# Optimization experiments

Hardware: AMD Instinct MI355X
Metric: run time of the kernel (lower is better)

Reference implementation:

```python
import jax, jax.numpy as jnp
import numpy as np

TAU = 1.0
LOSS_WEIGHT = 1.0
N = 4_000_000


def setup_inputs() -> dict:
    key = jax.random.key(0)
    k1, k2 = jax.random.split(key)

    def make_boxes(k):
        u = jax.random.uniform(k, (N, 5), dtype=jnp.float32)
        xy = u[:, :2] * 1024.0                 # centers in a 1024px image
        wh = u[:, 2:4] * 100.0 + 4.0           # box sizes in [4, 104)
        r = (u[:, 4:5] - 0.5) * jnp.pi         # angle in [-pi/2, pi/2)
        return jnp.concatenate([xy, wh, r], axis=-1)

    return {"pred": make_boxes(k1), "target": make_boxes(k2)}


def xy_wh_r_2_xy_sigma(xywhr):
    """(N,5) rbox -> (mu (N,2), sigma (N,2,2)) via R @ (S/2)^2 @ R^T closed form."""
    xy = xywhr[..., :2]
    wh = jnp.clip(xywhr[..., 2:4], 1e-7, 1e7)
    r = xywhr[..., 4]
    c, s = jnp.cos(r), jnp.sin(r)
    a = (0.5 * wh[..., 0]) ** 2  # (w/2)^2
    b = (0.5 * wh[..., 1]) ** 2  # (h/2)^2
    s00 = a * c * c + b * s * s
    s11 = a * s * s + b * c * c
    s01 = (a - b) * s * c
    sigma = jnp.stack(
        [jnp.stack([s00, s01], -1), jnp.stack([s01, s11], -1)], -2
    )  # (N,2,2)
    return xy, sigma


def _det2(m):
    return m[..., 0, 0] * m[..., 1, 1] - m[..., 0, 1] * m[..., 1, 0]


def _inv2(m):
    det = _det2(m)
    adj = jnp.stack(
        [jnp.stack([m[..., 1, 1], -m[..., 0, 1]], -1),
         jnp.stack([-m[..., 1, 0], m[..., 0, 0]], -1)], -2)
    return adj / det[..., None, None]


def kld_loss(mu_p, sigma_p, mu_t, sigma_t, tau):
    delta = mu_p - mu_t                                # (N,2)
    sigma_t_inv = _inv2(sigma_t)                       # (N,2,2)
    # delta^T Sigma_t^{-1} delta
    term1 = jnp.einsum('ni,nij,nj->n', delta, sigma_t_inv, delta)
    # tr(Sigma_t^{-1} Sigma_p) + log(det Sigma_t / det Sigma_p)
    tr = jnp.einsum('nij,nji->n', sigma_t_inv, sigma_p)
    term2 = tr + jnp.log(_det2(sigma_t) / _det2(sigma_p))
    dis = term1 + term2 - 2.0
    kl_dis = jnp.maximum(dis, 1e-6)
    # fun == 'log1p'
    loss = 1.0 - 1.0 / (tau + jnp.log1p(kl_dis))
    return loss[:, None]                               # (N,1) like torch version


def reference(pred, target):
    mu_p, sigma_p = xy_wh_r_2_xy_sigma(pred)
    mu_t, sigma_t = xy_wh_r_2_xy_sigma(target)
    return kld_loss(mu_p, sigma_p, mu_t, sigma_t, TAU) * LOSS_WEIGHT
```

## Files before the change

kernel.cpp:

```cpp
#include <hip/hip_runtime.h>
#include <math.h>

#ifndef TAU_CONST
#define TAU_CONST 1.0f
#endif

__device__ __forceinline__ void rbox_to_gauss(float x, float y, float w, float h, float r,
                                              float& mx, float& my,
                                              float& s00, float& s01, float& s11, float& det) {
    w = fminf(fmaxf(w, 1e-7f), 1e7f);
    h = fminf(fmaxf(h, 1e-7f), 1e7f);
    float a = 0.25f * w * w;
    float b = 0.25f * h * h;
    float s2, c2;
    __sincosf(r + r, &s2, &c2);
    float hs = 0.5f * (a + b);
    float hd = 0.5f * (a - b);
    s00 = fmaf(hd, c2, hs);
    s11 = fmaf(-hd, c2, hs);
    s01 = hd * s2;
    det = a * b;
    mx = x; my = y;
}

__device__ __forceinline__ float kld_row(const float* p, const float* t) {
    float pmx, pmy, p00, p01, p11, dp;
    float tmx, tmy, t00, t01, t11, dt;
    rbox_to_gauss(p[0], p[1], p[2], p[3], p[4], pmx, pmy, p00, p01, p11, dp);
    rbox_to_gauss(t[0], t[1], t[2], t[3], t[4], tmx, tmy, t00, t01, t11, dt);
    float dx = pmx - tmx, dy = pmy - tmy;
    float inv_dt = __builtin_amdgcn_rcpf(dt);
    float inv_dp = __builtin_amdgcn_rcpf(dp);
    float term1 = (dx * dx * t11 - 2.0f * dx * dy * t01 + dy * dy * t00) * inv_dt;
    float tr = (t11 * p00 + t00 * p11 - 2.0f * t01 * p01) * inv_dt;
    float term2 = tr + __logf(dt * inv_dp);
    float dis = term1 + term2 - 2.0f;
    float kl = fmaxf(dis, 1e-6f);
    float l1p = __logf(1.0f + kl);
    return 1.0f - __builtin_amdgcn_rcpf(TAU_CONST + l1p);
}

__global__ void __launch_bounds__(256) gdloss_vec4_kernel(const float* __restrict__ pred,
                                                          const float* __restrict__ target,
                                                          float* __restrict__ out, int n4) {
    int tid = blockIdx.x * blockDim.x + threadIdx.x;
    if (tid >= n4) return;
    const float4* pp = (const float4*)pred;
    const float4* tp = (const float4*)target;
    float4 pv[5], tv[5];
#pragma unroll
    for (int k = 0; k < 5; ++k) {
        pv[k] = pp[5 * tid + k];
        tv[k] = tp[5 * tid + k];
    }
    const float* pf = (const float*)pv;
    const float* tf = (const float*)tv;
    float4 o;
    o.x = kld_row(pf + 0,  tf + 0);
    o.y = kld_row(pf + 5,  tf + 5);
    o.z = kld_row(pf + 10, tf + 10);
    o.w = kld_row(pf + 15, tf + 15);
    ((float4*)out)[tid] = o;
}

__global__ void gdloss_tail_kernel(const float* __restrict__ pred,
                                   const float* __restrict__ target,
                                   float* __restrict__ out, int start, int n) {
    int i = start + blockIdx.x * blockDim.x + threadIdx.x;
    if (i >= n) return;
    float p[5], t[5];
#pragma unroll
    for (int k = 0; k < 5; ++k) {
        p[k] = pred[5 * i + k];
        t[k] = target[5 * i + k];
    }
    out[i] = kld_row(p, t);
}

extern "C" void kernel_launch(void* const* d_in, const int* in_sizes, int n_in,
                              void* d_out, int out_size, void* d_ws, size_t ws_size,
                              hipStream_t stream) {
    const float* pred   = (const float*)d_in[0];
    const float* target = (const float*)d_in[1];
    float* out = (float*)d_out;
    int n = in_sizes[0] / 5;
    int n4 = n / 4;
    if (n4 > 0) {
        int blocks = (n4 + 255) / 256;
        gdloss_vec4_kernel<<<blocks, 256, 0, stream>>>(pred, target, out, n4);
    }
    int rem = n - n4 * 4;
    if (rem > 0) {
        gdloss_tail_kernel<<<1, 64, 0, stream>>>(pred, target, out, n4 * 4, n);
    }
}
```

Baseline: 176.7 us.

## Stage inputs through LDS with coalesced direct global-to-LDS loads

Replaces per-thread strided float4 loads with wave-coalesced global_load_lds transfers into shared memory, then each thread reads two rows from LDS and writes a float2. This targets poor coalescing of the 20-byte row layout and register pressure from holding four rows per thread. It adds a block barrier and possible LDS bank conflicts on the 10-float stride reads, and widens the tail kernel launch.

```diff
diff --git a/kernel.cpp b/kernel.cpp
--- a/kernel.cpp
+++ b/kernel.cpp
@@ -1,9 +1,11 @@
 #include <hip/hip_runtime.h>
 #include <math.h>
+#include <stdint.h>
 
 #ifndef TAU_CONST
 #define TAU_CONST 1.0f
 #endif
+
 
 __device__ __forceinline__ void rbox_to_gauss(float x, float y, float w, float h, float r,
                                               float& mx, float& my,
@@ -40,27 +42,45 @@
     return 1.0f - __builtin_amdgcn_rcpf(TAU_CONST + l1p);
 }
 
-__global__ void __launch_bounds__(256) gdloss_vec4_kernel(const float* __restrict__ pred,
-                                                          const float* __restrict__ target,
-                                                          float* __restrict__ out, int n4) {
-    int tid = blockIdx.x * blockDim.x + threadIdx.x;
-    if (tid >= n4) return;
-    const float4* pp = (const float4*)pred;
-    const float4* tp = (const float4*)target;
-    float4 pv[5], tv[5];
+
+__device__ __forceinline__ void gload_lds16(const void* g, void* l) {
+    __builtin_amdgcn_global_load_lds((const __attribute__((address_space(1))) uint32_t*)g,
+                                     (__attribute__((address_space(3))) uint32_t*)l,
+                                     16, 0, 0);
+}
+
+__global__ void __launch_bounds__(256, 8) gdloss_lds_kernel(const float* __restrict__ pred,
+                                                            const float* __restrict__ target,
+                                                            float* __restrict__ out) {
+    __shared__ float lds[5120];
+    const int tid = threadIdx.x;
+    const int wv  = tid >> 6;
+    const int ln  = tid & 63;
+    const long long base = (long long)blockIdx.x * 2560;
+
 #pragma unroll
     for (int k = 0; k < 5; ++k) {
-        pv[k] = pp[5 * tid + k];
-        tv[k] = tp[5 * tid + k];
+        int c = wv * 5 + k;
+        const float* g = (c < 10) ? (pred   + base + c * 256 + ln * 4)
+                                  : (target + base + (c - 10) * 256 + ln * 4);
+        gload_lds16(g, &lds[c * 256]);
     }
-    const float* pf = (const float*)pv;
-    const float* tf = (const float*)tv;
-    float4 o;
-    o.x = kld_row(pf + 0,  tf + 0);
-    o.y = kld_row(pf + 5,  tf + 5);
-    o.z = kld_row(pf + 10, tf + 10);
-    o.w = kld_row(pf + 15, tf + 15);
-    ((float4*)out)[tid] = o;
+    __syncthreads();
+
+    const float2* lp = (const float2*)&lds[10 * tid];
+    const float2* lt = (const float2*)&lds[2560 + 10 * tid];
+    float2 p0 = lp[0], p1 = lp[1], p2 = lp[2], p3 = lp[3], p4 = lp[4];
+    float2 t0 = lt[0], t1 = lt[1], t2 = lt[2], t3 = lt[3], t4 = lt[4];
+
+    float pr0[5] = {p0.x, p0.y, p1.x, p1.y, p2.x};
+    float pr1[5] = {p2.y, p3.x, p3.y, p4.x, p4.y};
+    float tr0[5] = {t0.x, t0.y, t1.x, t1.y, t2.x};
+    float tr1[5] = {t2.y, t3.x, t3.y, t4.x, t4.y};
+
+    float2 o;
+    o.x = kld_row(pr0, tr0);
+    o.y = kld_row(pr1, tr1);
+    ((float2*)out)[(size_t)blockIdx.x * 256 + tid] = o;
 }
 
 __global__ void gdloss_tail_kernel(const float* __restrict__ pred,
@@ -83,14 +103,15 @@
     const float* pred   = (const float*)d_in[0];
     const float* target = (const float*)d_in[1];
     float* out = (float*)d_out;
-    int n = in_sizes[0] / 5;
-    int n4 = n / 4;
-    if (n4 > 0) {
-        int blocks = (n4 + 255) / 256;
-        gdloss_vec4_kernel<<<blocks, 256, 0, stream>>>(pred, target, out, n4);
+    int n  = in_sizes[0] / 5;
+    int nb = n / 512;
+    if (nb > 0) {
+        gdloss_lds_kernel<<<nb, 256, 0, stream>>>(pred, target, out);
     }
-    int rem = n - n4 * 4;
+    int start = nb * 512;
+    int rem = n - start;
     if (rem > 0) {
-        gdloss_tail_kernel<<<1, 64, 0, stream>>>(pred, target, out, n4 * 4, n);
+        int tb = (rem + 255) / 256;
+        gdloss_tail_kernel<<<tb, 256, 0, stream>>>(pred, target, out, start, n);
     }
 }
```

Measured after the change: 178.5 us. Within noise of the previous version (+1.0%).
